# Kernel tuning notes

Hardware: AMD Instinct MI355X
Metric: run time of the kernel (lower is better)

Reference implementation:

```python
import jax, jax.numpy as jnp
import numpy as np

MU = 23.359
STD = 1.41
Q_LIM = 500.0
DAY = 24.0 * 3600.0
WEEK = 7.0 * DAY


def setup_inputs() -> dict:
    key = jax.random.key(0)
    ks = jax.random.split(key, 6)
    n, n_rooms, h, T, n_tout = 256, 254, 64, 50000, 2048
    m = 1 + n_rooms  # u = [Tout, Q_per_room]
    t_eval = jnp.arange(T, dtype=jnp.float32) * 30.0
    # Hurwitz A: slow RC thermal dynamics (eigenvalues ~ -1e-4 1/s)
    A = 1e-4 * (0.3 * jax.random.normal(ks[0], (n, n), jnp.float32) / np.sqrt(n)
                - jnp.eye(n, dtype=jnp.float32))
    B = 1e-6 * jax.random.uniform(ks[1], (n, m), jnp.float32)
    cooling = jax.random.uniform(ks[2], (n_rooms, 1), jnp.float32)
    w1 = 0.05 * jax.random.normal(ks[3], (h, n + 4), jnp.float32)
    b1 = jnp.zeros((h,), jnp.float32)
    w2 = 0.1 * jax.random.normal(ks[4], (h,), jnp.float32)
    # outside-temperature interpolation table covering [0, T*30+30]
    tout_ts = jnp.linspace(0.0, float(T) * 30.0 + 30.0, n_tout, dtype=jnp.float32)
    tout_vals = 10.0 + 5.0 * jax.random.normal(ks[5], (n_tout,), jnp.float32)
    return dict(t_eval=t_eval, A=A, B=B, cooling=cooling, w1=w1, b1=b1, w2=w2,
                tout_ts=tout_ts, tout_vals=tout_vals)


def _integrate(t_eval, A, B, cooling, w1, b1, w2, tout_ts, tout_vals):
    n = A.shape[0]
    # transform=sigmoid then heat_scaling(Q_lim)
    heat = jax.nn.sigmoid(cooling[:, 0]) * Q_LIM  # [n_rooms]
    t0 = t_eval[0]
    ts = t_eval - t0
    dt = ts[1] - ts[0]
    iv = 26.0 * jnp.ones((n,), jnp.float32)

    def action_of(x, t):
        xn = (x - MU) / STD
        sig = jnp.stack([jnp.sin(t * (2.0 * jnp.pi / DAY)),
                         jnp.cos(t * (2.0 * jnp.pi / DAY)),
                         jnp.sin(t * (2.0 * jnp.pi / WEEK)),
                         jnp.cos(t * (2.0 * jnp.pi / WEEK))])
        s = jnp.concatenate([xn, sig])  # [n+4]
        return jax.nn.sigmoid(jnp.dot(w2, jnp.tanh(w1 @ s + b1)))  # scalar action

    def f(x, t, Q):
        # dy/dt = A x + B u,  u = [Tout(t+t0), Q]
        Tout = jnp.interp(t + t0, tout_ts, tout_vals)
        u = jnp.concatenate([Tout[None], Q])
        return A @ x + B @ u

    def step(x, t):
        # policy action held over the RK4 substeps (30 s policy hold == dt)
        Q = -heat * action_of(x, t)
        k1 = f(x, t, Q)
        k2 = f(x + 0.5 * dt * k1, t + 0.5 * dt, Q)
        k3 = f(x + 0.5 * dt * k2, t + 0.5 * dt, Q)
        k4 = f(x + dt * k3, t + dt, Q)
        x_new = x + (dt / 6.0) * (k1 + 2.0 * k2 + 2.0 * k3 + k4)
        return x_new, x  # emit state AT t (odeint returns iv first)

    _, traj = jax.lax.scan(step, iv, ts)
    return traj  # [T, n]


_integrate_jit = jax.jit(_integrate)


def reference(t_eval, A, B, cooling, w1, b1, w2, tout_ts, tout_vals):
    return _integrate_jit(t_eval, A, B, cooling, w1, b1, w2, tout_ts, tout_vals)
```

## Files before the change

### kernel.cpp

```cpp
#include <hip/hip_runtime.h>
#include <math.h>

#define NN 256
#define HH 64

typedef unsigned int uint32;
typedef _Float16 h2f __attribute__((ext_vector_type(2)));

__device__ __forceinline__ float sigm(float x) { return 1.0f / (1.0f + expf(-x)); }

__device__ __forceinline__ float dot2f(float a, uint32 b, float c) {
#if __has_builtin(__builtin_amdgcn_fdot2)
    return __builtin_amdgcn_fdot2(__builtin_bit_cast(h2f, a),
                                  __builtin_bit_cast(h2f, b), c, false);
#else
    h2f x = __builtin_bit_cast(h2f, a), y = __builtin_bit_cast(h2f, b);
    return c + (float)x[0] * (float)y[0] + (float)x[1] * (float)y[1];
#endif
}

__global__ void k_affine(const float* __restrict__ A, float* __restrict__ Pout,
                         const float* __restrict__ tev, int div)
{
    int i = blockIdx.x, j = threadIdx.x;
    double h = (double)tev[1] - (double)tev[0];
    double v = (i == j ? 1.0 : 0.0) + (h / (double)div) * (double)A[i * NN + j];
    Pout[i * NN + j] = (float)v;
}

__global__ void k_gemm(const float* __restrict__ A, const float* __restrict__ Pin,
                       float* __restrict__ Pout, const float* __restrict__ tev, int div)
{
    int i = blockIdx.x, j = threadIdx.x;
    double h = (double)tev[1] - (double)tev[0];
    const float* Ar = A + i * NN;
    double acc = 0.0;
    for (int k = 0; k < NN; ++k) acc += (double)Ar[k] * (double)Pin[k * NN + j];
    double v = (i == j ? 1.0 : 0.0) + (h / (double)div) * acc;
    Pout[i * NN + j] = (float)v;
}

__global__ void k_prep_vec(const float* __restrict__ A, const float* __restrict__ B,
                           const float* __restrict__ cooling, const float* __restrict__ tev,
                           const float* __restrict__ R, float* __restrict__ gq)
{
    __shared__ float heat[NN];
    __shared__ float vin[NN];
    int t = threadIdx.x;
    double h = (double)tev[1] - (double)tev[0];
    heat[t] = (t < NN - 2) ? 500.0f * sigm(cooling[t]) : 0.0f;
    __syncthreads();
    float B0 = B[t * (NN - 1)];
    double bh = 0.0;
    for (int j = 0; j < NN - 2; ++j) bh += (double)B[t * (NN - 1) + 1 + j] * (double)heat[j];
    vin[t] = B0; __syncthreads();
    double v1 = 0.0; for (int k = 0; k < NN; ++k) v1 += (double)A[t * NN + k] * (double)vin[k];
    __syncthreads(); vin[t] = (float)v1; __syncthreads();
    double v2 = 0.0; for (int k = 0; k < NN; ++k) v2 += (double)A[t * NN + k] * (double)vin[k];
    __syncthreads(); vin[t] = (float)v2; __syncthreads();
    double v3 = 0.0; for (int k = 0; k < NN; ++k) v3 += (double)A[t * NN + k] * (double)vin[k];
    __syncthreads();
    vin[t] = (float)bh; __syncthreads();
    double u1 = 0.0; for (int k = 0; k < NN; ++k) u1 += (double)A[t * NN + k] * (double)vin[k];
    __syncthreads(); vin[t] = (float)u1; __syncthreads();
    double u2 = 0.0; for (int k = 0; k < NN; ++k) u2 += (double)A[t * NN + k] * (double)vin[k];
    __syncthreads(); vin[t] = (float)u2; __syncthreads();
    double u3 = 0.0; for (int k = 0; k < NN; ++k) u3 += (double)A[t * NN + k] * (double)vin[k];

    double srow = 0.0;
    for (int c = 0; c < NN; ++c) srow += (double)R[t * NN + c];
    srow -= 1.0;

    gq[t]        = (float)((h / 6.0) * (double)B0);
    gq[256 + t]  = (float)((h * h / 6.0) * v1);
    gq[512 + t]  = (float)((h * h * h / 12.0) * v2);
    gq[768 + t]  = (float)((h * h * h * h / 24.0) * v3);
    gq[1024 + t] = (float)(h * bh + (h * h / 2.0) * u1 + (h * h * h / 6.0) * u2
                           + (h * h * h * h / 24.0) * u3);
    gq[1280 + t] = (float)(23.359 * srow);
}

__device__ __forceinline__ float interp1(float x, const float* __restrict__ ts,
                                         const float* __restrict__ vs, int n)
{
    int lo = 0, hi = n;
    while (lo < hi) { int mid = (lo + hi) >> 1; if (ts[mid] <= x) lo = mid + 1; else hi = mid; }
    int i = lo; if (i < 1) i = 1; if (i > n - 1) i = n - 1;
    float xim = ts[i - 1], xi = ts[i];
    float fim = vs[i - 1], fi = vs[i];
    return fim + (x - xim) / (xi - xim) * (fi - fim);
}

__global__ void k_time(const float* __restrict__ tev, const float* __restrict__ tts,
                       const float* __restrict__ tvals, float* __restrict__ td,
                       int T, int ntout)
{
    int k = blockIdx.x * blockDim.x + threadIdx.x;
    if (k >= T) return;
    float t0 = tev[0];
    float dtf = tev[1] - t0;
    float t = tev[k] - t0;
    const float cD = (float)(2.0 * M_PI / 86400.0);
    const float cW = (float)(2.0 * M_PI / 604800.0);
    float f0 = (float)sin((double)(t * cD));
    float f1 = (float)cos((double)(t * cD));
    float f2 = (float)sin((double)(t * cW));
    float f3 = (float)cos((double)(t * cW));
    float To1 = interp1(t + t0, tts, tvals, ntout);
    float To2 = interp1((t + 0.5f * dtf) + t0, tts, tvals, ntout);
    float To4 = interp1((t + dtf) + t0, tts, tvals, ntout);
    size_t o = (size_t)k * 8;
    td[o + 0] = To1 + 4.0f * To2 + To4;
    td[o + 1] = To1 + 2.0f * To2;
    td[o + 2] = To1 + To2;
    td[o + 3] = To1;
    td[o + 4] = f0; td[o + 5] = f1; td[o + 6] = f2; td[o + 7] = f3;
}

__global__ void k_packE(const float* __restrict__ R, uint32* __restrict__ Epk)
{
    int d = blockIdx.x * 256 + threadIdx.x;
    int r = d >> 7, i = d & 127;
    int c = 2 * i;
    float e0 = 64.0f * (R[r * NN + c]     - (r == c     ? 1.0f : 0.0f));
    float e1 = 64.0f * (R[r * NN + c + 1] - (r == c + 1 ? 1.0f : 0.0f));
    union { _Float16 h[2]; uint32 u; } p;
    p.h[0] = (_Float16)e0; p.h[1] = (_Float16)e1;
    Epk[d] = p.u;
}

__global__ void k_packW(const float* __restrict__ w1, uint32* __restrict__ w1pk)
{
    int d = blockIdx.x * 256 + threadIdx.x;
    int t = d >> 5, s = d & 31;
    int jr = t >> 2, c = t & 3;
    int j = s >> 2, q = s & 3;
    int col = 2 * (16 * j + 4 * c + q);
    const float is = 1.0f / 1.41f;
    union { _Float16 h[2]; uint32 u; } p;
    p.h[0] = (_Float16)(w1[jr * 260 + col] * is);
    p.h[1] = (_Float16)(w1[jr * 260 + col + 1] * is);
    w1pk[d] = p.u;
}

__global__ __launch_bounds__(256, 1) void k_main(
    const float* __restrict__ tdata, const float* Epk, const float* w1pk,
    const float* gq, const float* __restrict__ w1g,
    const float* __restrict__ b1g, const float* __restrict__ w2g,
    float* out, int T)
{
    __shared__ __align__(16) uint32 spk[132];
    __shared__ float wf[6 * HH];
    __shared__ float hid[HH];
    __shared__ float b1eff[HH];
    __shared__ float td[2][8];

    const int t = threadIdx.x;
    const int jr = t >> 2;
    const int c = t & 3;
    const int lane = t & 63;

    float4 Ereg[32];
    {
        const float4* Eg = reinterpret_cast<const float4*>(Epk) + (size_t)t * 32;
        #pragma unroll
        for (int i = 0; i < 32; ++i) Ereg[i] = Eg[i];
    }
    float4 Wreg[8];
    {
        const float4* Wg = reinterpret_cast<const float4*>(w1pk) + (size_t)t * 8;
        #pragma unroll
        for (int i = 0; i < 8; ++i) Wreg[i] = Wg[i];
    }
    float g0r = gq[t], g1r = gq[256 + t], g2r = gq[512 + t], g3r = gq[768 + t];
    float qr = gq[1024 + t], cer = gq[1280 + t];
    float w2r = w2g[lane];

    if (t < HH) {
        wf[t]       = w1g[t * 260 + 256];
        wf[64 + t]  = w1g[t * 260 + 257];
        wf[128 + t] = w1g[t * 260 + 258];
        wf[192 + t] = w1g[t * 260 + 259];
        wf[256 + t] = b1g[t];
        wf[320 + t] = w2g[t];
    }
    _Float16* sph = reinterpret_cast<_Float16*>(spk);
    float xr = 26.0f;
    sph[t] = (_Float16)(26.0f - 23.359f);
    if (t < 8) td[0][t] = tdata[t];
    __syncthreads();
    if (t < HH)
        b1eff[t] = wf[256 + t] + wf[t] * td[0][4] + wf[64 + t] * td[0][5]
                 + wf[128 + t] * td[0][6] + wf[192 + t] * td[0][7];
    __syncthreads();

    const uint4* sp4 = reinterpret_cast<const uint4*>(spk);

    for (int k = 0; k < T; ++k) {
        const int cur = k & 1, nxt = cur ^ 1;
        float tdp = 0.0f;
        if (t >= 248 && k + 1 < T) tdp = tdata[(size_t)(k + 1) * 8 + (t - 248)];

        float hs = 0.0f;
        {
            #pragma unroll
            for (int j = 0; j < 8; ++j) {
                uint4 sx = sp4[4 * j + c];
                float4 w = Wreg[j];
                hs = dot2f(w.x, sx.x, hs); hs = dot2f(w.y, sx.y, hs);
                hs = dot2f(w.z, sx.z, hs); hs = dot2f(w.w, sx.w, hs);
            }
        }
        hs += __shfl_xor(hs, 1); hs += __shfl_xor(hs, 2);
        if (c == 0) hid[jr] = tanhf(hs + b1eff[jr]);

        float ac0 = 0.f, ac1 = 0.f, ac2 = 0.f, ac3 = 0.f;
        {
            #pragma unroll
            for (int i = 0; i < 32; ++i) {
                uint4 xq = sp4[i];
                float4 e = Ereg[i];
                ac0 = dot2f(e.x, xq.x, ac0);
                ac1 = dot2f(e.y, xq.y, ac1);
                ac2 = dot2f(e.z, xq.z, ac2);
                ac3 = dot2f(e.w, xq.w, ac3);
            }
        }
        float y = (ac0 + ac1) + (ac2 + ac3);

        out[(size_t)k * NN + t] = xr;
        if (t >= 248) td[nxt][t - 248] = tdp;
        asm volatile("s_waitcnt lgkmcnt(0)\ns_barrier" ::: "memory");

        {
            float v = w2r * hid[lane];
            v += __shfl_xor(v, 1);  v += __shfl_xor(v, 2);  v += __shfl_xor(v, 4);
            v += __shfl_xor(v, 8);  v += __shfl_xor(v, 16); v += __shfl_xor(v, 32);
            float aS = sigm(v);
            float S0 = td[cur][0], S1 = td[cur][1], S2 = td[cur][2], S3 = td[cur][3];
            float xn = xr + y * 0.015625f + cer
                     + S0 * g0r + S1 * g1r + S2 * g2r + S3 * g3r - aS * qr;
            xr = xn;
            sph[t] = (_Float16)(xn - 23.359f);
        }
        if (t < HH && k + 1 < T)
            b1eff[t] = wf[256 + t] + wf[t] * td[nxt][4] + wf[64 + t] * td[nxt][5]
                     + wf[128 + t] * td[nxt][6] + wf[192 + t] * td[nxt][7];
        asm volatile("s_waitcnt lgkmcnt(0)\ns_barrier" ::: "memory");
    }
}

extern "C" void kernel_launch(void* const* d_in, const int* in_sizes, int n_in,
                              void* d_out, int out_size, void* d_ws, size_t ws_size,
                              hipStream_t stream)
{
    (void)n_in; (void)out_size; (void)ws_size;
    const float* tev     = (const float*)d_in[0];
    const float* A       = (const float*)d_in[1];
    const float* B       = (const float*)d_in[2];
    const float* cooling = (const float*)d_in[3];
    const float* w1      = (const float*)d_in[4];
    const float* b1      = (const float*)d_in[5];
    const float* w2      = (const float*)d_in[6];
    const float* tts     = (const float*)d_in[7];
    const float* tvals   = (const float*)d_in[8];
    const int T     = in_sizes[0];
    const int ntout = in_sizes[7];

    float* out = (float*)d_out;
    float* ws  = (float*)d_ws;
    float*  R    = ws;
    float*  gq   = ws + 65536;
    uint32* w1pk = (uint32*)(ws + 67072);
    float*  td   = ws + 75264;
    float* P1 = out;
    float* P2 = out + 65536;
    size_t outN = (size_t)T * NN;
    uint32* Epk = (uint32*)(out + outN - 32768);

    hipLaunchKernelGGL(k_affine, dim3(256), dim3(256), 0, stream, A, P1, tev, 4);
    hipLaunchKernelGGL(k_gemm,   dim3(256), dim3(256), 0, stream, A, P1, P2, tev, 3);
    hipLaunchKernelGGL(k_gemm,   dim3(256), dim3(256), 0, stream, A, P2, P1, tev, 2);
    hipLaunchKernelGGL(k_gemm,   dim3(256), dim3(256), 0, stream, A, P1, R,  tev, 1);
    hipLaunchKernelGGL(k_packE,  dim3(128), dim3(256), 0, stream, R, Epk);
    hipLaunchKernelGGL(k_packW,  dim3(32),  dim3(256), 0, stream, w1, w1pk);
    hipLaunchKernelGGL(k_prep_vec, dim3(1), dim3(256), 0, stream, A, B, cooling, tev, R, gq);
    hipLaunchKernelGGL(k_time, dim3((T + 255) / 256), dim3(256), 0, stream,
                       tev, tts, tvals, td, T, ntout);
    hipLaunchKernelGGL(k_main, dim3(1), dim3(256), 0, stream,
                       td, (const float*)Epk, (const float*)w1pk, gq, w1, b1, w2, out, T);
}
```

Baseline: 69.42 ms.

## Split per-step matvec across 1024 threads with readlane broadcast and partial sums

The single-block sequential integrator grows from 256 to 1024 threads. Each quarter of the threads computes a quarter of the fp16 state-matrix dot product and writes partial sums to shared memory, which the first 256 threads combine. The state vector is now broadcast with readlane instead of wide LDS reads, and the hidden-layer dot product is spread over 16 lanes per unit with tanh deferred to the combine phase. Each thread does less serial work per step, in exchange for more threads taking part in every barrier and an extra shared-memory reduction.

```diff
diff --git a/kernel.cpp b/kernel.cpp
--- a/kernel.cpp
+++ b/kernel.cpp
@@ -9,13 +9,21 @@
 
 __device__ __forceinline__ float sigm(float x) { return 1.0f / (1.0f + expf(-x)); }
 
-__device__ __forceinline__ float dot2f(float a, uint32 b, float c) {
+__device__ __forceinline__ float dot2(uint32 a, uint32 b, float c) {
 #if __has_builtin(__builtin_amdgcn_fdot2)
     return __builtin_amdgcn_fdot2(__builtin_bit_cast(h2f, a),
                                   __builtin_bit_cast(h2f, b), c, false);
 #else
     h2f x = __builtin_bit_cast(h2f, a), y = __builtin_bit_cast(h2f, b);
     return c + (float)x[0] * (float)y[0] + (float)x[1] * (float)y[1];
+#endif
+}
+
+__device__ __forceinline__ uint32 rdlane(uint32 v, int l) {
+#if __has_builtin(__builtin_amdgcn_readlane)
+    return (uint32)__builtin_amdgcn_readlane((int)v, l);
+#else
+    return (uint32)__shfl((int)v, l);
 #endif
 }
 
@@ -120,8 +128,9 @@
 __global__ void k_packE(const float* __restrict__ R, uint32* __restrict__ Epk)
 {
     int d = blockIdx.x * 256 + threadIdx.x;
-    int r = d >> 7, i = d & 127;
-    int c = 2 * i;
+    int t = d >> 5, i = d & 31;
+    int r = t & 255, qt = t >> 8;
+    int c = qt * 64 + 2 * i;
     float e0 = 64.0f * (R[r * NN + c]     - (r == c     ? 1.0f : 0.0f));
     float e1 = 64.0f * (R[r * NN + c + 1] - (r == c + 1 ? 1.0f : 0.0f));
     union { _Float16 h[2]; uint32 u; } p;
@@ -132,10 +141,9 @@
 __global__ void k_packW(const float* __restrict__ w1, uint32* __restrict__ w1pk)
 {
     int d = blockIdx.x * 256 + threadIdx.x;
-    int t = d >> 5, s = d & 31;
-    int jr = t >> 2, c = t & 3;
-    int j = s >> 2, q = s & 3;
-    int col = 2 * (16 * j + 4 * c + q);
+    int t = d >> 3, i = d & 7;
+    int jr = t >> 4, c = t & 15;
+    int col = 16 * c + 2 * i;
     const float is = 1.0f / 1.41f;
     union { _Float16 h[2]; uint32 u; } p;
     p.h[0] = (_Float16)(w1[jr * 260 + col] * is);
@@ -143,37 +151,47 @@
     w1pk[d] = p.u;
 }
 
-__global__ __launch_bounds__(256, 1) void k_main(
-    const float* __restrict__ tdata, const float* Epk, const float* w1pk,
-    const float* gq, const float* __restrict__ w1g,
-    const float* __restrict__ b1g, const float* __restrict__ w2g,
-    float* out, int T)
+__global__
+__attribute__((amdgpu_flat_work_group_size(1024, 1024)))
+__attribute__((amdgpu_waves_per_eu(4, 4)))
+void k_main(
+    const float* __restrict__ tdata, const uint32* Epk,
+    const uint32* __restrict__ w1pk, const float* __restrict__ gq,
+    const float* __restrict__ w1g, const float* __restrict__ b1g,
+    const float* __restrict__ w2g, float* out, int T)
 {
     __shared__ __align__(16) uint32 spk[132];
+    __shared__ __align__(16) float part[4][NN];
+    __shared__ float hspre[HH];
+    __shared__ float b1eff[2][HH];
     __shared__ float wf[6 * HH];
-    __shared__ float hid[HH];
-    __shared__ float b1eff[HH];
     __shared__ float td[2][8];
 
     const int t = threadIdx.x;
-    const int jr = t >> 2;
-    const int c = t & 3;
+    const int r = t & 255;
+    const int qt = t >> 8;
+    const int jr = t >> 4;
+    const int c  = t & 15;
     const int lane = t & 63;
 
-    float4 Ereg[32];
+    uint32 Ereg[32];
     {
-        const float4* Eg = reinterpret_cast<const float4*>(Epk) + (size_t)t * 32;
+        const uint4* Eg = reinterpret_cast<const uint4*>(Epk) + (size_t)t * 8;
         #pragma unroll
-        for (int i = 0; i < 32; ++i) Ereg[i] = Eg[i];
+        for (int i = 0; i < 8; ++i) {
+            uint4 v = Eg[i];
+            Ereg[4 * i + 0] = v.x; Ereg[4 * i + 1] = v.y;
+            Ereg[4 * i + 2] = v.z; Ereg[4 * i + 3] = v.w;
+        }
     }
-    float4 Wreg[8];
+    uint32 Wreg[8];
     {
-        const float4* Wg = reinterpret_cast<const float4*>(w1pk) + (size_t)t * 8;
-        #pragma unroll
-        for (int i = 0; i < 8; ++i) Wreg[i] = Wg[i];
+        const uint4* Wg = reinterpret_cast<const uint4*>(w1pk) + (size_t)t * 2;
+        uint4 v = Wg[0]; Wreg[0] = v.x; Wreg[1] = v.y; Wreg[2] = v.z; Wreg[3] = v.w;
+        v = Wg[1];       Wreg[4] = v.x; Wreg[5] = v.y; Wreg[6] = v.z; Wreg[7] = v.w;
     }
-    float g0r = gq[t], g1r = gq[256 + t], g2r = gq[512 + t], g3r = gq[768 + t];
-    float qr = gq[1024 + t], cer = gq[1280 + t];
+    float g0r = gq[r], g1r = gq[256 + r], g2r = gq[512 + r], g3r = gq[768 + r];
+    float qr = gq[1024 + r], cer = gq[1280 + r];
     float w2r = w2g[lane];
 
     if (t < HH) {
@@ -186,12 +204,12 @@
     }
     _Float16* sph = reinterpret_cast<_Float16*>(spk);
     float xr = 26.0f;
-    sph[t] = (_Float16)(26.0f - 23.359f);
+    if (t < NN) sph[t] = (_Float16)(26.0f - 23.359f);
     if (t < 8) td[0][t] = tdata[t];
     __syncthreads();
     if (t < HH)
-        b1eff[t] = wf[256 + t] + wf[t] * td[0][4] + wf[64 + t] * td[0][5]
-                 + wf[128 + t] * td[0][6] + wf[192 + t] * td[0][7];
+        b1eff[0][t] = wf[256 + t] + wf[t] * td[0][4] + wf[64 + t] * td[0][5]
+                    + wf[128 + t] * td[0][6] + wf[192 + t] * td[0][7];
     __syncthreads();
 
     const uint4* sp4 = reinterpret_cast<const uint4*>(spk);
@@ -199,53 +217,56 @@
     for (int k = 0; k < T; ++k) {
         const int cur = k & 1, nxt = cur ^ 1;
         float tdp = 0.0f;
-        if (t >= 248 && k + 1 < T) tdp = tdata[(size_t)(k + 1) * 8 + (t - 248)];
+        if (t >= 1016 && k + 1 < T) tdp = tdata[(size_t)(k + 1) * 8 + (t - 1016)];
 
         float hs = 0.0f;
         {
-            #pragma unroll
-            for (int j = 0; j < 8; ++j) {
-                uint4 sx = sp4[4 * j + c];
-                float4 w = Wreg[j];
-                hs = dot2f(w.x, sx.x, hs); hs = dot2f(w.y, sx.y, hs);
-                hs = dot2f(w.z, sx.z, hs); hs = dot2f(w.w, sx.w, hs);
-            }
+            uint4 s0 = sp4[c * 2], s1 = sp4[c * 2 + 1];
+            hs = dot2(Wreg[0], s0.x, hs); hs = dot2(Wreg[1], s0.y, hs);
+            hs = dot2(Wreg[2], s0.z, hs); hs = dot2(Wreg[3], s0.w, hs);
+            hs = dot2(Wreg[4], s1.x, hs); hs = dot2(Wreg[5], s1.y, hs);
+            hs = dot2(Wreg[6], s1.z, hs); hs = dot2(Wreg[7], s1.w, hs);
         }
         hs += __shfl_xor(hs, 1); hs += __shfl_xor(hs, 2);
-        if (c == 0) hid[jr] = tanhf(hs + b1eff[jr]);
-
+        hs += __shfl_xor(hs, 4); hs += __shfl_xor(hs, 8);
+        if (c == 0) hspre[jr] = hs;
+
+        uint32 xld = spk[qt * 32 + (lane & 31)];
         float ac0 = 0.f, ac1 = 0.f, ac2 = 0.f, ac3 = 0.f;
-        {
-            #pragma unroll
-            for (int i = 0; i < 32; ++i) {
-                uint4 xq = sp4[i];
-                float4 e = Ereg[i];
-                ac0 = dot2f(e.x, xq.x, ac0);
-                ac1 = dot2f(e.y, xq.y, ac1);
-                ac2 = dot2f(e.z, xq.z, ac2);
-                ac3 = dot2f(e.w, xq.w, ac3);
-            }
+        #pragma unroll
+        for (int i = 0; i < 8; ++i) {
+            uint32 u0 = rdlane(xld, 4 * i + 0);
+            uint32 u1 = rdlane(xld, 4 * i + 1);
+            uint32 u2 = rdlane(xld, 4 * i + 2);
+            uint32 u3 = rdlane(xld, 4 * i + 3);
+            ac0 = dot2(Ereg[4 * i + 0], u0, ac0);
+            ac1 = dot2(Ereg[4 * i + 1], u1, ac1);
+            ac2 = dot2(Ereg[4 * i + 2], u2, ac2);
+            ac3 = dot2(Ereg[4 * i + 3], u3, ac3);
         }
-        float y = (ac0 + ac1) + (ac2 + ac3);
-
-        out[(size_t)k * NN + t] = xr;
-        if (t >= 248) td[nxt][t - 248] = tdp;
+        part[qt][r] = (ac0 + ac1) + (ac2 + ac3);
+
+        if (t < NN) out[(size_t)k * NN + t] = xr;
+        if (t >= 1016) td[nxt][t - 1016] = tdp;
         asm volatile("s_waitcnt lgkmcnt(0)\ns_barrier" ::: "memory");
 
-        {
-            float v = w2r * hid[lane];
+        if (t < NN) {
+            float h = tanhf(hspre[lane] + b1eff[cur][lane]);
+            float v = w2r * h;
             v += __shfl_xor(v, 1);  v += __shfl_xor(v, 2);  v += __shfl_xor(v, 4);
             v += __shfl_xor(v, 8);  v += __shfl_xor(v, 16); v += __shfl_xor(v, 32);
             float aS = sigm(v);
             float S0 = td[cur][0], S1 = td[cur][1], S2 = td[cur][2], S3 = td[cur][3];
-            float xn = xr + y * 0.015625f + cer
+            float y = ((part[0][t] + part[1][t]) + (part[2][t] + part[3][t])) * 0.015625f;
+            float xn = xr + y + cer
                      + S0 * g0r + S1 * g1r + S2 * g2r + S3 * g3r - aS * qr;
             xr = xn;
             sph[t] = (_Float16)(xn - 23.359f);
+        } else if (t < 320 && k + 1 < T) {
+            int j = t - 256;
+            b1eff[nxt][j] = wf[256 + j] + wf[j] * td[nxt][4] + wf[64 + j] * td[nxt][5]
+                          + wf[128 + j] * td[nxt][6] + wf[192 + j] * td[nxt][7];
         }
-        if (t < HH && k + 1 < T)
-            b1eff[t] = wf[256 + t] + wf[t] * td[nxt][4] + wf[64 + t] * td[nxt][5]
-                     + wf[128 + t] * td[nxt][6] + wf[192 + t] * td[nxt][7];
         asm volatile("s_waitcnt lgkmcnt(0)\ns_barrier" ::: "memory");
     }
 }
@@ -287,6 +308,6 @@
     hipLaunchKernelGGL(k_prep_vec, dim3(1), dim3(256), 0, stream, A, B, cooling, tev, R, gq);
     hipLaunchKernelGGL(k_time, dim3((T + 255) / 256), dim3(256), 0, stream,
                        tev, tts, tvals, td, T, ntout);
-    hipLaunchKernelGGL(k_main, dim3(1), dim3(256), 0, stream,
-                       td, (const float*)Epk, (const float*)w1pk, gq, w1, b1, w2, out, T);
-}
+    hipLaunchKernelGGL(k_main, dim3(1), dim3(1024), 0, stream,
+                       td, Epk, w1pk, gq, w1, b1, w2, out, T);
+}
```

Result: faster. 68.06 ms (-2.0%).
